# Performance work log

Measured on AMD Instinct MI355X. Metric: run time of the kernel, lower is better.

Reference implementation:

```python
import jax, jax.numpy as jnp
import numpy as np

EMBED_DIM = 1024
NUM_HEADS = 16
HEAD_DIM = EMBED_DIM // NUM_HEADS


def setup_inputs() -> dict:
    key = jax.random.key(0)
    ks = jax.random.split(key, 9)
    B, S, E = 2, 2048, EMBED_DIM
    lim = 1.0 / np.sqrt(E)
    def lin(kw, kb):
        W = jax.random.uniform(kw, (E, E), jnp.float32, -lim, lim)
        b = jax.random.uniform(kb, (E,), jnp.float32, -lim, lim)
        return W, b
    Wq, bq = lin(ks[0], ks[1])
    Wk, bk = lin(ks[2], ks[3])
    Wv, bv = lin(ks[4], ks[5])
    Wo, bo = lin(ks[6], ks[7])
    x = jax.random.normal(ks[8], (B, S, E), jnp.float32)
    return {"x": x, "Wq": Wq, "bq": bq, "Wk": Wk, "bk": bk,
            "Wv": Wv, "bv": bv, "Wo": Wo, "bo": bo}


def reference(x, Wq, bq, Wk, bk, Wv, bv, Wo, bo):
    B, S, E = x.shape
    H, D = NUM_HEADS, HEAD_DIM
    scale = D ** -0.5
    # projections (torch Linear: x @ W.T + b); here W stored as [in, out]-equivalent via transpose convention
    q = (x @ Wq.T + bq).reshape(B, S, H, D).transpose(0, 2, 1, 3)  # b h s d
    k = (x @ Wk.T + bk).reshape(B, S, H, D).transpose(0, 2, 1, 3)
    v = (x @ Wv.T + bv).reshape(B, S, H, D).transpose(0, 2, 1, 3)
    scores = jnp.einsum('bhqd,bhkd->bhqk', q, k) * scale
    attn = jax.nn.softmax(scores, axis=-1)
    out = jnp.einsum('bhqk,bhkd->bhqd', attn, v)
    out = out.transpose(0, 2, 1, 3).reshape(B, S, E)
    return out @ Wo.T + bo
```

## Files before the change

### kernel.cpp

```cpp
#include <hip/hip_runtime.h>


using u16 = unsigned short;
using u32 = unsigned int;

typedef __bf16 bf16x8 __attribute__((ext_vector_type(8)));
typedef float  f32x4  __attribute__((ext_vector_type(4)));
typedef float  f32x16 __attribute__((ext_vector_type(16)));
typedef u32    u32x4  __attribute__((ext_vector_type(4)));

constexpr int GB = 2;
constexpr int GS = 2048;
constexpr int GH = 16;
constexpr int GD = 64;
constexpr int GE = 1024;
constexpr int GM = GB * GS;
constexpr int PSTRIDE = 2048;
constexpr float SCQ = 0.125f * 1.44269504088896f;

__device__ __forceinline__ u16 f2bf(float f) {
    u32 u = __float_as_uint(f);
    u += 0x7FFFu + ((u >> 16) & 1u);
    return (u16)(u >> 16);
}

__device__ __forceinline__ void plswap(u32& a, u32& b) {
#if __has_builtin(__builtin_amdgcn_permlane32_swap)
    auto r = __builtin_amdgcn_permlane32_swap(a, b, false, false);
    a = r[0]; b = r[1];
#else
    asm volatile("v_permlane32_swap_b32 %0, %1" : "+v"(a), "+v"(b));
#endif
}

__device__ __forceinline__ float xchg32(float v) {
    u32 a = __float_as_uint(v), b = a;
    plswap(a, b);
    return __uint_as_float((threadIdx.x & 32) ? a : b);
}

__device__ __forceinline__ u32 cvtpk(float lo, float hi) {
    u32 d;
    asm("v_cvt_pk_bf16_f32 %0, %1, %2" : "=v"(d) : "v"(lo), "v"(hi));
    return d;
}

__device__ __forceinline__ void gl_lds16(const u16* g, u16* l) {
#if __has_builtin(__builtin_amdgcn_global_load_lds)
    __builtin_amdgcn_global_load_lds(
        (const __attribute__((address_space(1))) void*)g,
        (__attribute__((address_space(3))) void*)l, 16, 0, 0);
#else
    *reinterpret_cast<uint4*>(l) = *reinterpret_cast<const uint4*>(g);
#endif
}

__global__ void cvt_all(const float* __restrict__ x,
                        const float* __restrict__ w1, const float* __restrict__ w2,
                        const float* __restrict__ w3, const float* __restrict__ w4,
                        u16* __restrict__ ox,
                        u16* __restrict__ o1, u16* __restrict__ o2,
                        u16* __restrict__ o3, u16* __restrict__ o4) {
    const int y = blockIdx.y;
    const float* in = y == 0 ? x : y == 1 ? w1 : y == 2 ? w2 : y == 3 ? w3 : w4;
    u16* out = y == 0 ? ox : y == 1 ? o1 : y == 2 ? o2 : y == 3 ? o3 : o4;
    const int n = y == 0 ? GM * GE : GE * GE;
    int idx = blockIdx.x * blockDim.x + threadIdx.x;
    int stride = gridDim.x * blockDim.x;
    for (int i = idx * 4; i < n; i += stride * 4) {
        float4 f = *reinterpret_cast<const float4*>(in + i);
        ushort4 o;
        o.x = f2bf(f.x); o.y = f2bf(f.y); o.z = f2bf(f.z); o.w = f2bf(f.w);
        *reinterpret_cast<ushort4*>(out + i) = o;
    }
}

__global__ __launch_bounds__(256)
void qkv_gemm(const u16* __restrict__ A,
              const u16* __restrict__ wq, const u16* __restrict__ wk, const u16* __restrict__ wv,
              const float* __restrict__ bq, const float* __restrict__ bk, const float* __restrict__ bv,
              u16* __restrict__ Qb, u16* __restrict__ Kb, u16* __restrict__ VTb) {
    constexpr int Kd = GE;
    __shared__ u16 As[128 * 32];
    __shared__ u16 Bs[128 * 32];

    const int z = blockIdx.z;
    const u16* __restrict__ Bw = z == 0 ? wq : z == 1 ? wk : wv;
    const float* __restrict__ bias = z == 0 ? bq : z == 1 ? bk : bv;
    u16* __restrict__ outp = z == 0 ? Qb : z == 1 ? Kb : VTb;
    const float oscale = z == 0 ? SCQ : 1.0f;

    const int tid = threadIdx.x;
    const int m0 = blockIdx.y * 128;
    const int n0 = blockIdx.x * 128;
    const int wave = tid >> 6, lane = tid & 63;
    const int wm = (wave >> 1) * 64, wn = (wave & 1) * 64;
    const int g = lane >> 4, rw = lane & 15;

    f32x4 acc[4][4] = {};

    for (int kt = 0; kt < Kd; kt += 32) {
        __syncthreads();
#pragma unroll
        for (int j = 0; j < 2; ++j) {
            int c = wave * 128 + j * 64 + lane;
            int r = c >> 2, u = (c & 3) * 8;
            gl_lds16(&A [(size_t)(m0 + r) * Kd + kt + u], &As[c * 8]);
            gl_lds16(&Bw[(size_t)(n0 + r) * Kd + kt + u], &Bs[c * 8]);
        }
        __syncthreads();

        bf16x8 aF[4], bF[4];
#pragma unroll
        for (int mf = 0; mf < 4; ++mf)
            aF[mf] = *reinterpret_cast<const bf16x8*>(&As[(wm + mf * 16 + rw) * 32 + g * 8]);
#pragma unroll
        for (int nf = 0; nf < 4; ++nf)
            bF[nf] = *reinterpret_cast<const bf16x8*>(&Bs[(wn + nf * 16 + rw) * 32 + g * 8]);
#pragma unroll
        for (int mf = 0; mf < 4; ++mf)
#pragma unroll
            for (int nf = 0; nf < 4; ++nf)
                acc[mf][nf] = __builtin_amdgcn_mfma_f32_16x16x32_bf16(aF[mf], bF[nf], acc[mf][nf], 0, 0, 0);
    }

#pragma unroll
    for (int mf = 0; mf < 4; ++mf)
#pragma unroll
        for (int nf = 0; nf < 4; ++nf)
#pragma unroll
            for (int r = 0; r < 4; ++r) {
                int m = m0 + wm + mf * 16 + g * 4 + r;
                int n = n0 + wn + nf * 16 + rw;
                u16 hv = f2bf((acc[mf][nf][r] + bias[n]) * oscale);
                int b = m >> 11, s = m & (GS - 1);
                int h = n >> 6, d = n & 63;
                if (z == 2)
                    outp[(((size_t)(b * GH + h)) * GD + d) * GS + s] = hv;
                else
                    outp[(((size_t)(b * GH + h)) * GS + s) * GD + d] = hv;
            }
}

__global__ __launch_bounds__(256)
void out_gemm(const u16* __restrict__ A, const u16* __restrict__ Bw,
              const float* __restrict__ bias, float* __restrict__ outp) {
    constexpr int Kd = GE, Nd = GE;
    __shared__ u16 As[128 * 32];
    __shared__ u16 Bs[64 * 32];

    const int m0 = blockIdx.y * 128;
    const int n0 = blockIdx.x * 64;

    const int tid = threadIdx.x;
    const int wave = tid >> 6, lane = tid & 63;
    const int wm = (wave >> 1) * 64, wn = (wave & 1) * 32;
    const int g = lane >> 4, rw = lane & 15;

    f32x4 acc[4][2] = {};

    for (int kt = 0; kt < Kd; kt += 32) {
        __syncthreads();
        {
            int c = tid;
            int r = c >> 2, u = (c & 3) * 8;
            gl_lds16(&A [(size_t)(m0 + r) * Kd + kt + u], &As[c * 8]);
            int c2 = tid + 256;
            int r2 = c2 >> 2, u2 = (c2 & 3) * 8;
            gl_lds16(&A [(size_t)(m0 + r2) * Kd + kt + u2], &As[c2 * 8]);
            gl_lds16(&Bw[(size_t)(n0 + r) * Kd + kt + u], &Bs[c * 8]);
        }
        __syncthreads();

        bf16x8 aF[4], bF[2];
#pragma unroll
        for (int mf = 0; mf < 4; ++mf)
            aF[mf] = *reinterpret_cast<const bf16x8*>(&As[(wm + mf * 16 + rw) * 32 + g * 8]);
#pragma unroll
        for (int nf = 0; nf < 2; ++nf)
            bF[nf] = *reinterpret_cast<const bf16x8*>(&Bs[(wn + nf * 16 + rw) * 32 + g * 8]);
#pragma unroll
        for (int mf = 0; mf < 4; ++mf)
#pragma unroll
            for (int nf = 0; nf < 2; ++nf)
                acc[mf][nf] = __builtin_amdgcn_mfma_f32_16x16x32_bf16(aF[mf], bF[nf], acc[mf][nf], 0, 0, 0);
    }

#pragma unroll
    for (int mf = 0; mf < 4; ++mf)
#pragma unroll
        for (int nf = 0; nf < 2; ++nf)
#pragma unroll
            for (int r = 0; r < 4; ++r) {
                int m = m0 + wm + mf * 16 + g * 4 + r;
                int n = n0 + wn + nf * 16 + rw;
                outp[(size_t)m * Nd + n] = acc[mf][nf][r] + bias[n];
            }
}

template <int NSPLIT>
__global__ __launch_bounds__(512)
void attn_kernel(const u16* __restrict__ Q, const u16* __restrict__ Kp,
                 const u16* __restrict__ VT, u16* __restrict__ ctx,
                 float* __restrict__ Opart, float* __restrict__ Lpart) {
    int bh, qb, split;
    if (NSPLIT == 2) {
        const int wg = (blockIdx.x & 7) * 64 + (blockIdx.x >> 3);
        bh = wg >> 4;
        split = wg & 1;
        qb = ((wg >> 1) & 7) * 256;
    } else {
        const int wg = (blockIdx.x & 7) * 32 + (blockIdx.x >> 3);
        bh = wg >> 3;
        split = 0;
        qb = (wg & 7) * 256;
    }
    const int tid = threadIdx.x;
    const int wave = tid >> 6;
    const int lane = tid & 63;
    const int l31 = lane & 31;
    const int hi = (lane >> 5) & 1;
    const int q0 = qb + wave * 32;
    constexpr int KVLEN = GS / NSPLIT;
    constexpr int NT = KVLEN / 128;
    const int kvbase = split * KVLEN;

    const u16* __restrict__ Qbh = Q  + (size_t)bh * GS * GD;
    const u16* __restrict__ Kbh = Kp + (size_t)bh * GS * GD;
    const u16* __restrict__ Vbh = VT + (size_t)bh * GD * GS;

    __shared__ u16 sK[2][8192];
    __shared__ u16 sV[2][8192];

    bf16x8 qf[4];
#pragma unroll
    for (int s = 0; s < 4; ++s)
        qf[s] = *reinterpret_cast<const bf16x8*>(
            Qbh + (size_t)(q0 + l31) * GD + hi * 8 + 16 * s);

    f32x16 O0 = {}, O1 = {};
    float lsum = 0.f;

    const int kr0 = tid >> 3, kw0 = tid & 7;
    const u16* kSrc = Kbh + (size_t)(kvbase + kr0) * GD + ((kw0 ^ (kr0 & 7)) * 8);
    const int vr0 = tid >> 4, vw0 = tid & 15;
    const int vcol = ((vw0 & 8) | ((vw0 & 7) ^ (vr0 & 7))) * 8;
    const u16* vSrc = Vbh + (size_t)vr0 * GS + kvbase + vcol;
    u16* const dK0 = &sK[0][tid * 8];
    u16* const dK1 = &sK[1][tid * 8];
    u16* const dV0 = &sV[0][tid * 8];
    u16* const dV1 = &sV[1][tid * 8];

    auto stageTo = [&](u16* dk, u16* dv, const u16* ks, const u16* vs) {
        gl_lds16(ks,           dk);
        gl_lds16(ks + 64 * GD, dk + 4096);
        gl_lds16(vs,           dv);
        gl_lds16(vs + 32 * GS, dv + 4096);
    };

    int offK[4], offV[4];
#pragma unroll
    for (int s = 0; s < 4; ++s) {
        int sw = ((2 * s + hi) ^ (l31 & 7)) * 8;
        offK[s] = l31 * 64 + sw;
        offV[s] = l31 * 128 + sw;
    }

    auto half = [&](const u16* bK, const u16* bV) {
        f32x16 sa = {}, sb = {};
        bf16x8 ka[4], kb[4];
#pragma unroll
        for (int s = 0; s < 4; ++s) {
            ka[s] = *reinterpret_cast<const bf16x8*>(&bK[offK[s]]);
            kb[s] = *reinterpret_cast<const bf16x8*>(&bK[offK[s] + 2048]);
        }
        __builtin_amdgcn_s_setprio(1);
#pragma unroll
        for (int s = 0; s < 4; ++s) {
            sa = __builtin_amdgcn_mfma_f32_32x32x16_bf16(ka[s], qf[s], sa, 0, 0, 0);
            sb = __builtin_amdgcn_mfma_f32_32x32x16_bf16(kb[s], qf[s], sb, 0, 0, 0);
        }
        __builtin_amdgcn_s_setprio(0);

        bf16x8 vf0[4], vf1[4];
#pragma unroll
        for (int s = 0; s < 4; ++s) {
            vf0[s] = *reinterpret_cast<const bf16x8*>(&bV[offV[s]]);
            vf1[s] = *reinterpret_cast<const bf16x8*>(&bV[offV[s] + 4096]);
        }

        float pa[16], pb[16];
#pragma unroll
        for (int r = 0; r < 16; ++r) {
            pa[r] = __builtin_amdgcn_exp2f(sa[r]);
            pb[r] = __builtin_amdgcn_exp2f(sb[r]);
        }
        float s16[16];
#pragma unroll
        for (int r = 0; r < 16; ++r) s16[r] = pa[r] + pb[r];
#pragma unroll
        for (int r = 0; r < 8; ++r) s16[r] += s16[r + 8];
#pragma unroll
        for (int r = 0; r < 4; ++r) s16[r] += s16[r + 4];
        lsum += (s16[0] + s16[1]) + (s16[2] + s16[3]);

        u32 wa[8], wb[8];
#pragma unroll
        for (int i = 0; i < 8; ++i) {
            wa[i] = cvtpk(pa[2 * i], pa[2 * i + 1]);
            wb[i] = cvtpk(pb[2 * i], pb[2 * i + 1]);
        }
        plswap(wa[0], wa[2]); plswap(wa[1], wa[3]);
        plswap(wa[4], wa[6]); plswap(wa[5], wa[7]);
        plswap(wb[0], wb[2]); plswap(wb[1], wb[3]);
        plswap(wb[4], wb[6]); plswap(wb[5], wb[7]);
        u32x4 a0 = {wa[0], wa[1], wa[2], wa[3]};
        u32x4 a1 = {wa[4], wa[5], wa[6], wa[7]};
        u32x4 b0 = {wb[0], wb[1], wb[2], wb[3]};
        u32x4 b1 = {wb[4], wb[5], wb[6], wb[7]};
        bf16x8 pva0 = __builtin_bit_cast(bf16x8, a0);
        bf16x8 pva1 = __builtin_bit_cast(bf16x8, a1);
        bf16x8 pvb0 = __builtin_bit_cast(bf16x8, b0);
        bf16x8 pvb1 = __builtin_bit_cast(bf16x8, b1);

        __builtin_amdgcn_s_setprio(1);
        O0 = __builtin_amdgcn_mfma_f32_32x32x16_bf16(vf0[0], pva0, O0, 0, 0, 0);
        O0 = __builtin_amdgcn_mfma_f32_32x32x16_bf16(vf0[1], pva1, O0, 0, 0, 0);
        O0 = __builtin_amdgcn_mfma_f32_32x32x16_bf16(vf0[2], pvb0, O0, 0, 0, 0);
        O0 = __builtin_amdgcn_mfma_f32_32x32x16_bf16(vf0[3], pvb1, O0, 0, 0, 0);
        O1 = __builtin_amdgcn_mfma_f32_32x32x16_bf16(vf1[0], pva0, O1, 0, 0, 0);
        O1 = __builtin_amdgcn_mfma_f32_32x32x16_bf16(vf1[1], pva1, O1, 0, 0, 0);
        O1 = __builtin_amdgcn_mfma_f32_32x32x16_bf16(vf1[2], pvb0, O1, 0, 0, 0);
        O1 = __builtin_amdgcn_mfma_f32_32x32x16_bf16(vf1[3], pvb1, O1, 0, 0, 0);
        __builtin_amdgcn_s_setprio(0);
    };

    stageTo(dK0, dV0, kSrc, vSrc);
    kSrc += 128 * GD; vSrc += 128;
    __syncthreads();

#pragma unroll 1
    for (int t = 0; t < NT; t += 2) {
        stageTo(dK1, dV1, kSrc, vSrc);
        kSrc += 128 * GD; vSrc += 128;
        half(sK[0], sV[0]);
        half(sK[0] + 4096, sV[0] + 64);
        __syncthreads();
        if (t + 2 < NT) {
            stageTo(dK0, dV0, kSrc, vSrc);
            kSrc += 128 * GD; vSrc += 128;
        }
        half(sK[1], sV[1]);
        half(sK[1] + 4096, sV[1] + 64);
        __syncthreads();
    }

    lsum += xchg32(lsum);

    if (NSPLIT > 1) {
        const int wt = bh * 64 + (q0 >> 5);
        const size_t base = ((size_t)wt * NSPLIT + split) * PSTRIDE;
#pragma unroll
        for (int r = 0; r < 16; ++r) {
            int d = (r & 3) + 8 * (r >> 2) + 4 * hi;
            Opart[base + (size_t)d * 32 + l31]        = O0[r];
            Opart[base + (size_t)(d + 32) * 32 + l31] = O1[r];
        }
        if (hi == 0)
            Lpart[(wt * NSPLIT + split) * 32 + l31] = lsum;
    } else {
        const int bb = bh >> 4, h = bh & 15;
        const float inv = 1.0f / lsum;
        u16* crow = ctx + ((size_t)(bb * GS + q0 + l31)) * GE + h * 64;
#pragma unroll
        for (int g2 = 0; g2 < 4; ++g2) {
            ushort4 st0, st1;
            st0.x = f2bf(O0[4 * g2 + 0] * inv); st0.y = f2bf(O0[4 * g2 + 1] * inv);
            st0.z = f2bf(O0[4 * g2 + 2] * inv); st0.w = f2bf(O0[4 * g2 + 3] * inv);
            st1.x = f2bf(O1[4 * g2 + 0] * inv); st1.y = f2bf(O1[4 * g2 + 1] * inv);
            st1.z = f2bf(O1[4 * g2 + 2] * inv); st1.w = f2bf(O1[4 * g2 + 3] * inv);
            *reinterpret_cast<ushort4*>(crow + 8 * g2 + 4 * hi)      = st0;
            *reinterpret_cast<ushort4*>(crow + 32 + 8 * g2 + 4 * hi) = st1;
        }
    }
}

template <int NSPLIT>
__global__ __launch_bounds__(256)
void combine_kernel(const float* __restrict__ Opart, const float* __restrict__ Lpart,
                    u16* __restrict__ ctx) {
    const int wt = blockIdx.x;
    const int bh = wt >> 6, bb = bh >> 4, h = bh & 15;
    const int q0 = (wt & 63) * 32;
    const int q = threadIdx.x & 31, db = threadIdx.x >> 5;
    const size_t b0 = (size_t)wt * NSPLIT * PSTRIDE;

    float lt = 0.f;
#pragma unroll
    for (int s = 0; s < NSPLIT; ++s) lt += Lpart[(wt * NSPLIT + s) * 32 + q];
    float inv = 1.f / lt;

    u16* crow = ctx + ((size_t)(bb * GS + q0 + q)) * GE + h * 64 + db * 8;
    ushort4 s0, s1;
    float o[8];
#pragma unroll
    for (int i = 0; i < 8; ++i) {
        int d = db * 8 + i;
        float acc = 0.f;
#pragma unroll
        for (int s = 0; s < NSPLIT; ++s)
            acc += Opart[b0 + (size_t)s * PSTRIDE + (size_t)d * 32 + q];
        o[i] = acc * inv;
    }
    s0.x = f2bf(o[0]); s0.y = f2bf(o[1]); s0.z = f2bf(o[2]); s0.w = f2bf(o[3]);
    s1.x = f2bf(o[4]); s1.y = f2bf(o[5]); s1.z = f2bf(o[6]); s1.w = f2bf(o[7]);
    *reinterpret_cast<ushort4*>(crow)     = s0;
    *reinterpret_cast<ushort4*>(crow + 4) = s1;
}

extern "C" void kernel_launch(void* const* d_in, const int* in_sizes, int n_in,
                              void* d_out, int out_size, void* d_ws, size_t ws_size,
                              hipStream_t stream) {
    (void)in_sizes; (void)n_in; (void)out_size;

    const float* x  = (const float*)d_in[0];
    const float* Wq = (const float*)d_in[1];
    const float* bq = (const float*)d_in[2];
    const float* Wk = (const float*)d_in[3];
    const float* bk = (const float*)d_in[4];
    const float* Wv = (const float*)d_in[5];
    const float* bv = (const float*)d_in[6];
    const float* Wo = (const float*)d_in[7];
    const float* bo = (const float*)d_in[8];
    float* out = (float*)d_out;

    char* ws = (char*)d_ws;
    u16* xb  = (u16*)(ws);
    u16* wqb = (u16*)(ws + (8ll  << 20));
    u16* wkb = (u16*)(ws + (10ll << 20));
    u16* wvb = (u16*)(ws + (12ll << 20));
    u16* wob = (u16*)(ws + (14ll << 20));
    u16* Qb  = (u16*)(ws + (16ll << 20));
    u16* Kb  = (u16*)(ws + (24ll << 20));
    u16* VTb = (u16*)(ws + (32ll << 20));
    u16* ctx = (u16*)(ws + (40ll << 20));
    float* Opart = (float*)(ws + (48ll << 20));
    float* Lpart = (float*)(ws + (80ll << 20));
    const bool split2 = ws_size >= (81ll << 20);

    cvt_all<<<dim3(1024, 5), 256, 0, stream>>>(x, Wq, Wk, Wv, Wo,
                                               xb, wqb, wkb, wvb, wob);

    qkv_gemm<<<dim3(GE / 128, GM / 128, 3), 256, 0, stream>>>(
        xb, wqb, wkb, wvb, bq, bk, bv, Qb, Kb, VTb);

    if (split2) {
        attn_kernel<2><<<dim3(512), 512, 0, stream>>>(Qb, Kb, VTb, ctx, Opart, Lpart);
        combine_kernel<2><<<dim3(2048), 256, 0, stream>>>(Opart, Lpart, ctx);
    } else {
        attn_kernel<1><<<dim3(256), 512, 0, stream>>>(Qb, Kb, VTb, ctx, Opart, Lpart);
    }

    out_gemm<<<dim3(GE / 64, GM / 128), 256, 0, stream>>>(ctx, wob, bo, out);
}
```

Measured before the change: 120.6 us.

## Double-buffer LDS tiles in QKV and output projection GEMMs

Both projection GEMMs now use two shared-memory buffers per operand. The next K tile is loaded asynchronously while MFMAs run on the current one, and the loop is unrolled by two with one barrier per half-step. This is meant to hide global-to-LDS load latency and drop one barrier per tile. In exchange, LDS use doubles per block, which can lower occupancy. The code also relies on the barrier ordering being correct for the async direct-to-LDS loads.

```diff
diff --git a/kernel.cpp b/kernel.cpp
--- a/kernel.cpp
+++ b/kernel.cpp
@@ -81,8 +81,8 @@
               const float* __restrict__ bq, const float* __restrict__ bk, const float* __restrict__ bv,
               u16* __restrict__ Qb, u16* __restrict__ Kb, u16* __restrict__ VTb) {
     constexpr int Kd = GE;
-    __shared__ u16 As[128 * 32];
-    __shared__ u16 Bs[128 * 32];
+    __shared__ u16 As[2][4096];
+    __shared__ u16 Bs[2][4096];
 
     const int z = blockIdx.z;
     const u16* __restrict__ Bw = z == 0 ? wq : z == 1 ? wk : wv;
@@ -99,29 +99,41 @@
 
     f32x4 acc[4][4] = {};
 
-    for (int kt = 0; kt < Kd; kt += 32) {
-        __syncthreads();
+    auto stage = [&](int b, int kt) {
 #pragma unroll
         for (int j = 0; j < 2; ++j) {
             int c = wave * 128 + j * 64 + lane;
             int r = c >> 2, u = (c & 3) * 8;
-            gl_lds16(&A [(size_t)(m0 + r) * Kd + kt + u], &As[c * 8]);
-            gl_lds16(&Bw[(size_t)(n0 + r) * Kd + kt + u], &Bs[c * 8]);
-        }
-        __syncthreads();
-
+            gl_lds16(&A [(size_t)(m0 + r) * Kd + kt + u], &As[b][c * 8]);
+            gl_lds16(&Bw[(size_t)(n0 + r) * Kd + kt + u], &Bs[b][c * 8]);
+        }
+    };
+
+    auto compute = [&](int b) {
         bf16x8 aF[4], bF[4];
 #pragma unroll
         for (int mf = 0; mf < 4; ++mf)
-            aF[mf] = *reinterpret_cast<const bf16x8*>(&As[(wm + mf * 16 + rw) * 32 + g * 8]);
+            aF[mf] = *reinterpret_cast<const bf16x8*>(&As[b][(wm + mf * 16 + rw) * 32 + g * 8]);
 #pragma unroll
         for (int nf = 0; nf < 4; ++nf)
-            bF[nf] = *reinterpret_cast<const bf16x8*>(&Bs[(wn + nf * 16 + rw) * 32 + g * 8]);
+            bF[nf] = *reinterpret_cast<const bf16x8*>(&Bs[b][(wn + nf * 16 + rw) * 32 + g * 8]);
 #pragma unroll
         for (int mf = 0; mf < 4; ++mf)
 #pragma unroll
             for (int nf = 0; nf < 4; ++nf)
                 acc[mf][nf] = __builtin_amdgcn_mfma_f32_16x16x32_bf16(aF[mf], bF[nf], acc[mf][nf], 0, 0, 0);
+    };
+
+    stage(0, 0);
+    __syncthreads();
+#pragma unroll 1
+    for (int kt = 0; kt < Kd; kt += 64) {
+        stage(1, kt + 32);
+        compute(0);
+        __syncthreads();
+        if (kt + 64 < Kd) stage(0, kt + 64);
+        compute(1);
+        __syncthreads();
     }
 
 #pragma unroll
@@ -146,8 +158,8 @@
 void out_gemm(const u16* __restrict__ A, const u16* __restrict__ Bw,
               const float* __restrict__ bias, float* __restrict__ outp) {
     constexpr int Kd = GE, Nd = GE;
-    __shared__ u16 As[128 * 32];
-    __shared__ u16 Bs[64 * 32];
+    __shared__ u16 As[2][4096];
+    __shared__ u16 Bs[2][2048];
 
     const int m0 = blockIdx.y * 128;
     const int n0 = blockIdx.x * 64;
@@ -159,31 +171,41 @@
 
     f32x4 acc[4][2] = {};
 
-    for (int kt = 0; kt < Kd; kt += 32) {
-        __syncthreads();
-        {
-            int c = tid;
-            int r = c >> 2, u = (c & 3) * 8;
-            gl_lds16(&A [(size_t)(m0 + r) * Kd + kt + u], &As[c * 8]);
-            int c2 = tid + 256;
-            int r2 = c2 >> 2, u2 = (c2 & 3) * 8;
-            gl_lds16(&A [(size_t)(m0 + r2) * Kd + kt + u2], &As[c2 * 8]);
-            gl_lds16(&Bw[(size_t)(n0 + r) * Kd + kt + u], &Bs[c * 8]);
-        }
-        __syncthreads();
-
+    auto stage = [&](int b, int kt) {
+        int c = tid;
+        int r = c >> 2, u = (c & 3) * 8;
+        gl_lds16(&A [(size_t)(m0 + r) * Kd + kt + u], &As[b][c * 8]);
+        int c2 = tid + 256;
+        int r2 = c2 >> 2, u2 = (c2 & 3) * 8;
+        gl_lds16(&A [(size_t)(m0 + r2) * Kd + kt + u2], &As[b][c2 * 8]);
+        gl_lds16(&Bw[(size_t)(n0 + r) * Kd + kt + u], &Bs[b][c * 8]);
+    };
+
+    auto compute = [&](int b) {
         bf16x8 aF[4], bF[2];
 #pragma unroll
         for (int mf = 0; mf < 4; ++mf)
-            aF[mf] = *reinterpret_cast<const bf16x8*>(&As[(wm + mf * 16 + rw) * 32 + g * 8]);
+            aF[mf] = *reinterpret_cast<const bf16x8*>(&As[b][(wm + mf * 16 + rw) * 32 + g * 8]);
 #pragma unroll
         for (int nf = 0; nf < 2; ++nf)
-            bF[nf] = *reinterpret_cast<const bf16x8*>(&Bs[(wn + nf * 16 + rw) * 32 + g * 8]);
+            bF[nf] = *reinterpret_cast<const bf16x8*>(&Bs[b][(wn + nf * 16 + rw) * 32 + g * 8]);
 #pragma unroll
         for (int mf = 0; mf < 4; ++mf)
 #pragma unroll
             for (int nf = 0; nf < 2; ++nf)
                 acc[mf][nf] = __builtin_amdgcn_mfma_f32_16x16x32_bf16(aF[mf], bF[nf], acc[mf][nf], 0, 0, 0);
+    };
+
+    stage(0, 0);
+    __syncthreads();
+#pragma unroll 1
+    for (int kt = 0; kt < Kd; kt += 64) {
+        stage(1, kt + 32);
+        compute(0);
+        __syncthreads();
+        if (kt + 64 < Kd) stage(0, kt + 64);
+        compute(1);
+        __syncthreads();
     }
 
 #pragma unroll
```

Measured after the change: 138.5 us. 1.15x slower.
